# Kernel tuning notes

Hardware: AMD Instinct MI355X
Metric: run time of the kernel (lower is better)

The kernel has to match this reference:

```python
import jax, jax.numpy as jnp
import numpy as np
from jax import lax

B, D, T = 8, 768, 1024
H = 8
DH = D // H  # 96
FF = 4 * D
NUM_BUCKETS = 320
HALF = NUM_BUCKETS // 2      # 160
SMALL = HALF // 2            # 80
MAX_DIST = 800
CONV_K = 31
ATTN_SCALE = 32.0


def setup_inputs() -> dict:
    key = jax.random.key(0)
    ks = jax.random.split(key, 32)
    n = lambda i, shape, s=0.02: jax.random.normal(ks[i], shape, dtype=jnp.float32) * s
    return {
        "x": jax.random.normal(ks[0], (B, D, T), dtype=jnp.float32),
        # ff1
        "w_ff1a": n(1, (D, FF)), "b_ff1a": jnp.zeros((FF,)),
        "w_ff1b": n(2, (FF, D)), "b_ff1b": jnp.zeros((D,)),
        # attention
        "w_qkv": n(3, (D, 3 * D)), "b_qkv": jnp.zeros((3 * D,)),
        "w_out": n(4, (D, D)), "b_out": jnp.zeros((D,)),
        # gated relative position bias
        "rel_embed": n(5, (NUM_BUCKETS, H), 1.0),
        "gate_u": n(6, (H, DH)), "gate_w": n(7, (H, DH)),
        "gate_scale": jnp.ones((H,)),
        # conv module
        "gn1_w": jnp.ones((D,)), "gn1_b": jnp.zeros((D,)),
        "pw1_w": n(8, (2 * D, D)), "pw1_b": jnp.zeros((2 * D,)),
        "dw_w": n(9, (D, CONV_K)), "dw_b": jnp.zeros((D,)),
        "gn2_w": jnp.ones((D,)), "gn2_b": jnp.zeros((D,)),
        "pw2_w": n(10, (D, D)), "pw2_b": jnp.zeros((D,)),
        # ff2
        "w_ff2a": n(11, (D, FF)), "b_ff2a": jnp.zeros((FF,)),
        "w_ff2b": n(12, (FF, D)), "b_ff2b": jnp.zeros((D,)),
    }


def _rel_buckets(seq_len):
    pos = jnp.arange(seq_len)
    rp = pos[None, :] - pos[:, None]              # [T, T]
    sign = (rp >= 0).astype(jnp.int32)
    ra = jnp.abs(rp)
    is_small = ra < SMALL
    rc = jnp.maximum(ra, 1)
    log_ratio = jnp.log(rc.astype(jnp.float32) / SMALL) / np.float32(np.log(MAX_DIST / SMALL))
    log_pos = SMALL + (log_ratio * (HALF - SMALL)).astype(jnp.int32)  # trunc toward zero like .long()
    log_pos = jnp.minimum(log_pos, HALF - 1)
    bucket = jnp.where(is_small, ra, log_pos) + sign * HALF
    return jnp.clip(bucket, 0, NUM_BUCKETS - 1)


def _groupnorm1(xc, w, b, eps=1e-5):
    # GroupNorm(1, C): normalize over (C, T) per sample; xc: [B, C, T]
    m = xc.mean(axis=(1, 2), keepdims=True)
    v = xc.var(axis=(1, 2), keepdims=True)
    return (xc - m) * lax.rsqrt(v + eps) * w[None, :, None] + b[None, :, None]


def reference(x, w_ff1a, b_ff1a, w_ff1b, b_ff1b, w_qkv, b_qkv, w_out, b_out,
              rel_embed, gate_u, gate_w, gate_scale,
              gn1_w, gn1_b, pw1_w, pw1_b, dw_w, dw_b, gn2_w, gn2_b, pw2_w, pw2_b,
              w_ff2a, b_ff2a, w_ff2b, b_ff2b):
    b_, d_, t_ = x.shape
    s = jnp.swapaxes(x, 1, 2)                          # [B, T, D]

    ff = lambda t, wa, ba, wb, bb: jax.nn.gelu(t @ wa + ba, approximate=False) @ wb + bb
    s = s + 0.5 * ff(s, w_ff1a, b_ff1a, w_ff1b, b_ff1b)

    qkv = (s @ w_qkv + b_qkv).reshape(b_, t_, 3, H, DH)
    q = jnp.swapaxes(qkv[:, :, 0], 1, 2)               # [B, H, T, DH]
    k = jnp.swapaxes(qkv[:, :, 1], 1, 2)
    v = jnp.swapaxes(qkv[:, :, 2], 1, 2)

    # WavLM-style rescaled scores
    scores = jnp.einsum('bhtd,bhsd->bhts', q / ATTN_SCALE, k)
    scores = (scores - scores.max(axis=-1, keepdims=True)) * ATTN_SCALE
    scores = scores / np.float32(np.sqrt(DH))

    # gated relative position bias
    buckets = _rel_buckets(t_)                          # [T, T]
    dtab = jnp.transpose(rel_embed[buckets], (2, 0, 1))[None]  # [1, H, T, T]
    g_u = jax.nn.sigmoid(jnp.einsum('bhtd,hd->bht', q, gate_u))[..., None]  # [B,H,T,1]
    g_r = jax.nn.sigmoid(jnp.einsum('bhtd,hd->bht', q, gate_w))[..., None]
    r_tilde = gate_scale[None, :, None, None] * g_r * dtab
    rel_bias = dtab + g_u * dtab + (1.0 - g_u) * r_tilde

    probs = jax.nn.softmax(scores + rel_bias, axis=-1)
    attn = jnp.einsum('bhts,bhsd->bhtd', probs, v)
    attn = jnp.swapaxes(attn, 1, 2).reshape(b_, t_, d_)
    s = s + attn @ w_out + b_out

    # conv module
    c = jnp.swapaxes(s, 1, 2)                           # [B, D, T]
    h = _groupnorm1(c, gn1_w, gn1_b)
    h = jnp.einsum('od,bdt->bot', pw1_w, h) + pw1_b[None, :, None]  # 1x1 conv -> [B, 2D, T]
    a, g = jnp.split(h, 2, axis=1)
    h = a * jax.nn.sigmoid(g)                           # GLU over channels
    h = lax.conv_general_dilated(h, dw_w[:, None, :], (1,), [(CONV_K // 2, CONV_K // 2)],
                                 feature_group_count=d_,
                                 dimension_numbers=('NCH', 'OIH', 'NCH')) + dw_b[None, :, None]
    h = jax.nn.silu(_groupnorm1(h, gn2_w, gn2_b))
    h = jnp.einsum('od,bdt->bot', pw2_w, h) + pw2_b[None, :, None]
    c = c + h

    ct = jnp.swapaxes(c, 1, 2)
    s = ct + 0.5 * ff(ct, w_ff2a, b_ff2a, w_ff2b, b_ff2b)
    return jnp.swapaxes(s, 1, 2)                        # [B, D, T]
```

## Files before the change

kernel.cpp:

```cpp
#include <hip/hip_runtime.h>
#include <hip/hip_bf16.h>
#include <cstdint>

typedef __attribute__((ext_vector_type(8))) __bf16 bf16x8;
typedef __attribute__((ext_vector_type(4))) float f32x4;
typedef unsigned short u16t;

constexpr int Bn = 8, Dn = 768, Tn = 1024, Hn = 8, DHn = 96, FFn = 3072;
constexpr int BT = Bn * Tn;
constexpr float INV_SQRT_DH = 0.10206207261596575f;

#define GLDS16(gp, lp) __builtin_amdgcn_global_load_lds( \
    (__attribute__((address_space(1))) unsigned int*)(uintptr_t)(gp), \
    (__attribute__((address_space(3))) unsigned int*)(uintptr_t)(lp), 16, 0, 0)

__global__ void k_prep(const float* __restrict__ w_ff1a, const float* __restrict__ w_ff1b,
                       const float* __restrict__ w_qkv, const float* __restrict__ w_out,
                       const float* __restrict__ w_ff2a, const float* __restrict__ w_ff2b,
                       const float* __restrict__ pw1_w, const float* __restrict__ pw2_w,
                       const float* __restrict__ rel_embed,
                       __hip_bfloat16* __restrict__ Wf1a, __hip_bfloat16* __restrict__ Wf1b,
                       __hip_bfloat16* __restrict__ Wqkv, __hip_bfloat16* __restrict__ Wout,
                       __hip_bfloat16* __restrict__ Wf2a, __hip_bfloat16* __restrict__ Wf2b,
                       __hip_bfloat16* __restrict__ Wpw1, __hip_bfloat16* __restrict__ Wpw2,
                       float* __restrict__ rel_tab) {
  __shared__ float t[32][33];
  const int tid = threadIdx.x;
  int bid = blockIdx.x;

  const float* tsrc = nullptr;
  __hip_bfloat16* tdst = nullptr;
  int K = 0, N = 0;
  if (bid < 2304) { tsrc = w_ff1a; tdst = Wf1a; K = 768; N = 3072; }
  else if ((bid -= 2304) < 2304) { tsrc = w_ff1b; tdst = Wf1b; K = 3072; N = 768; }
  else if ((bid -= 2304) < 1728) { tsrc = w_qkv; tdst = Wqkv; K = 768; N = 2304; }
  else if ((bid -= 1728) < 576)  { tsrc = w_out; tdst = Wout; K = 768; N = 768; }
  else if ((bid -= 576) < 2304)  { tsrc = w_ff2a; tdst = Wf2a; K = 768; N = 3072; }
  else if ((bid -= 2304) < 2304) { tsrc = w_ff2b; tdst = Wf2b; K = 3072; N = 768; }
  else {
    bid -= 2304;
    if (bid < 1152) {
      int i4 = bid * 1024 + tid * 4;
      int n = i4 / 768, k = i4 - n * 768;
      int on = (n >> 1) + (n & 1) * 768;
      float4 v = *(const float4*)(pw1_w + (size_t)on * 768 + k);
      __hip_bfloat16* d = Wpw1 + i4;
      d[0] = __float2bfloat16(v.x); d[1] = __float2bfloat16(v.y);
      d[2] = __float2bfloat16(v.z); d[3] = __float2bfloat16(v.w);
    } else if ((bid -= 1152) < 576) {
      int i4 = bid * 1024 + tid * 4;
      float4 v = *(const float4*)(pw2_w + i4);
      __hip_bfloat16* d = Wpw2 + i4;
      d[0] = __float2bfloat16(v.x); d[1] = __float2bfloat16(v.y);
      d[2] = __float2bfloat16(v.z); d[3] = __float2bfloat16(v.w);
    } else {
      bid -= 576;
      int dd = bid * 256 + tid;
      if (dd < 2047) {
        int d = dd - 1023;
        int sign = d >= 0 ? 1 : 0;
        int ra = d < 0 ? -d : d;
        int base;
        if (ra < 80) base = ra;
        else {
          float lr = logf((float)ra / 80.0f) / 2.3025851f;
          int lp = 80 + (int)(lr * 80.0f);
          base = lp < 159 ? lp : 159;
        }
        int bucket = base + sign * 160;
        if (bucket < 0) bucket = 0;
        if (bucket > 319) bucket = 319;
        for (int h = 0; h < 8; ++h)
          rel_tab[h * 2047 + dd] = rel_embed[bucket * 8 + h];
      }
    }
    return;
  }
  int nb32 = N / 32;
  int nb = (bid % nb32) * 32, kb = (bid / nb32) * 32;
  int tx = tid & 31, ty = tid >> 5;
  for (int i = ty; i < 32; i += 8)
    t[i][tx] = tsrc[(size_t)(kb + i) * N + nb + tx];
  __syncthreads();
  for (int i = ty; i < 32; i += 8)
    tdst[(size_t)(nb + i) * K + kb + tx] = __float2bfloat16(t[tx][i]);
}

__global__ void k_tin(const float* __restrict__ x, float* __restrict__ s,
                      __hip_bfloat16* __restrict__ sb) {
  __shared__ float t[32][33];
  int b = blockIdx.z;
  int t0 = blockIdx.x * 32, d0 = blockIdx.y * 32;
  int tx = threadIdx.x, ty = threadIdx.y;
  for (int i = ty; i < 32; i += 8)
    t[i][tx] = x[((size_t)b * Dn + d0 + i) * Tn + t0 + tx];
  __syncthreads();
  for (int i = ty; i < 32; i += 8) {
    float v = t[tx][i];
    size_t o = (size_t)(b * Tn + t0 + i) * Dn + d0 + tx;
    s[o] = v;
    sb[o] = __float2bfloat16(v);
  }
}

__global__ void k_tout(const float* __restrict__ s, float* __restrict__ out) {
  __shared__ float t[32][33];
  int b = blockIdx.z;
  int t0 = blockIdx.x * 32, d0 = blockIdx.y * 32;
  int tx = threadIdx.x, ty = threadIdx.y;
  for (int i = ty; i < 32; i += 8)
    t[i][tx] = s[(size_t)(b * Tn + t0 + i) * Dn + d0 + tx];
  __syncthreads();
  for (int i = ty; i < 32; i += 8)
    out[((size_t)b * Dn + d0 + i) * Tn + t0 + tx] = t[tx][i];
}

__global__ void k_vtrans(const __hip_bfloat16* __restrict__ qkv,
                         __hip_bfloat16* __restrict__ VT) {
  __shared__ __hip_bfloat16 t[32][33];
  int bh = blockIdx.z;
  int b = bh >> 3, h = bh & 7;
  int t0 = blockIdx.x * 32, d0 = blockIdx.y * 32;
  int tx = threadIdx.x, ty = threadIdx.y;
  for (int i = ty; i < 32; i += 8)
    t[i][tx] = qkv[(size_t)(b * Tn + t0 + i) * 2304 + 1536 + h * 96 + d0 + tx];
  __syncthreads();
  for (int i = ty; i < 32; i += 8)
    VT[((size_t)bh * 96 + d0 + i) * Tn + t0 + tx] = t[tx][i];
}

enum { EPI_BIAS = 0, EPI_GELU = 1, EPI_HALF_RES = 2, EPI_RES = 3, EPI_GLU = 4 };

template <int BM, int BN, int EPI>
__global__ __launch_bounds__(256)
void k_gemm(const __hip_bfloat16* __restrict__ A, const __hip_bfloat16* __restrict__ Bt,
            const float* __restrict__ bias, const float* __restrict__ resid,
            float* __restrict__ outF, __hip_bfloat16* __restrict__ outB,
            int M, int N, int K) {
  constexpr int MI = BM / 32;
  constexpr int NI = BN / 32;
  __shared__ __align__(16) __hip_bfloat16 lA[2][BM * 32];
  __shared__ __align__(16) __hip_bfloat16 lB[2][BN * 32];
  const int tid = threadIdx.x;
  const int lane = tid & 63, wv = tid >> 6;
  const int g = lane >> 4, c15 = lane & 15;
  const int gx = gridDim.x;
  const int nwg = gx * gridDim.y;
  const int orig = blockIdx.y * gx + blockIdx.x;
  const int q = nwg >> 3, rr = nwg & 7;
  const int xcd = orig & 7, idx = orig >> 3;
  const int wg = (xcd < rr ? xcd * (q + 1) : rr * (q + 1) + (xcd - rr) * q) + idx;
  const int m0 = (wg / gx) * BM, n0 = (wg % gx) * BN;
  const int wm = (wv >> 1) * (BM / 2), wn = (wv & 1) * (BN / 2);

  const int srow = lane >> 2, scol = (lane & 3) * 8;

  f32x4 acc[MI][NI] = {};

  auto stage = [&](int buf, int kt) {
#pragma unroll
    for (int c = 0; c < BM / 64; ++c) {
      int cid = wv * (BM / 64) + c;
      GLDS16(A + (size_t)(m0 + cid * 16 + srow) * K + kt + scol, &lA[buf][cid * 512]);
    }
#pragma unroll
    for (int c = 0; c < BN / 64; ++c) {
      int cid = wv * (BN / 64) + c;
      GLDS16(Bt + (size_t)(n0 + cid * 16 + srow) * K + kt + scol, &lB[buf][cid * 512]);
    }
  };

  const int nt = K >> 5;
  stage(0, 0);
  __syncthreads();
  int cur = 0;
  for (int t = 0; t < nt; ++t) {
    if (t + 1 < nt) stage(cur ^ 1, (t + 1) * 32);
    bf16x8 af[MI], bfr[NI];
#pragma unroll
    for (int i = 0; i < MI; ++i)
      af[i] = *(const bf16x8*)&lA[cur][(wm + i * 16 + c15) * 32 + g * 8];
#pragma unroll
    for (int j = 0; j < NI; ++j)
      bfr[j] = *(const bf16x8*)&lB[cur][(wn + j * 16 + c15) * 32 + g * 8];
#pragma unroll
    for (int i = 0; i < MI; ++i)
#pragma unroll
      for (int j = 0; j < NI; ++j)
        acc[i][j] = __builtin_amdgcn_mfma_f32_16x16x32_bf16(af[i], bfr[j], acc[i][j], 0, 0, 0);
    __syncthreads();
    cur ^= 1;
  }

#pragma unroll
  for (int i = 0; i < MI; ++i) {
    int row0 = m0 + wm + i * 16 + g * 4;
#pragma unroll
    for (int j = 0; j < NI; ++j) {
      int col = n0 + wn + j * 16 + c15;
      int bcol = (EPI == EPI_GLU) ? ((col >> 1) + (col & 1) * 768) : col;
      float bb = bias[bcol];
#pragma unroll
      for (int r = 0; r < 4; ++r) {
        int row = row0 + r;
        float v = acc[i][j][r] + bb;
        if (EPI == EPI_GELU) v = 0.5f * v * (1.0f + erff(v * 0.70710678118f));
        else if (EPI == EPI_HALF_RES) v = resid[(size_t)row * N + col] + 0.5f * v;
        else if (EPI == EPI_RES) v = resid[(size_t)row * N + col] + v;
        if (EPI == EPI_GLU) {
          float partner = __shfl_xor(v, 1);
          if (!(c15 & 1))
            outF[(size_t)row * (N >> 1) + (col >> 1)] =
                v * (1.0f / (1.0f + __expf(-partner)));
        } else {
          size_t o = (size_t)row * N + col;
          if (outF) outF[o] = v;
          if (outB) outB[o] = __float2bfloat16(v);
        }
      }
    }
  }
}

__global__ __launch_bounds__(256)
void k_attn(const __hip_bfloat16* __restrict__ qkv, const __hip_bfloat16* __restrict__ VT,
            const float* __restrict__ rel_tab,
            const float* __restrict__ gate_u, const float* __restrict__ gate_w,
            const float* __restrict__ gate_scale, __hip_bfloat16* __restrict__ ao) {
  __shared__ __align__(16) char smem[48128];
  __hip_bfloat16* kT = (__hip_bfloat16*)smem;
  __hip_bfloat16* vT = (__hip_bfloat16*)(smem + 13312);
  __hip_bfloat16* qT = (__hip_bfloat16*)(smem + 30208);
  __hip_bfloat16* pT = (__hip_bfloat16*)(smem + 30208);
  float* relLocal = (float*)(smem + 43520);
  float* cRow = (float*)(smem + 47872);

  const int tid = threadIdx.x, lane = tid & 63, wv = tid >> 6;
  const int g = lane >> 4, c15 = lane & 15;
  const int orig = blockIdx.y * 16 + blockIdx.x;
  const int wg = (orig & 7) * 128 + (orig >> 3);
  const int qt = wg & 15;
  const int bh = wg >> 4;
  const int b = bh >> 3, h = bh & 7;
  const int t0 = qt * 64;

  for (int i = tid; i < 1087; i += 256)
    relLocal[i] = rel_tab[h * 2047 + i + 960 - t0];

  {
    int r = tid >> 2, q4 = tid & 3;
    const __hip_bfloat16* src = qkv + (size_t)(b * Tn + t0 + r) * 2304 + h * 96 + q4 * 24;
    uint4 v0 = *(const uint4*)(src);
    uint4 v1 = *(const uint4*)(src + 8);
    uint4 v2 = *(const uint4*)(src + 16);
    *(uint4*)&qT[r * 104 + q4 * 24] = v0;
    *(uint4*)&qT[r * 104 + q4 * 24 + 8] = v1;
    *(uint4*)&qT[r * 104 + q4 * 24 + 16] = v2;
  }
  __syncthreads();

  if (tid < 64) {
    float du = 0.f, dw = 0.f;
#pragma unroll
    for (int c = 0; c < 12; ++c) {
      bf16x8 qv = *(const bf16x8*)&qT[tid * 104 + c * 8];
#pragma unroll
      for (int e = 0; e < 8; ++e) {
        float f = (float)qv[e];
        du += f * gate_u[h * 96 + c * 8 + e];
        dw += f * gate_w[h * 96 + c * 8 + e];
      }
    }
    float gu = 1.0f / (1.0f + __expf(-du));
    float gr = 1.0f / (1.0f + __expf(-dw));
    cRow[tid] = 1.0f + gu + (1.0f - gu) * gate_scale[h] * gr;
  }

  bf16x8 aQ[3];
#pragma unroll
  for (int c = 0; c < 3; ++c)
    aQ[c] = *(const bf16x8*)&qT[(wv * 16 + c15) * 104 + c * 32 + g * 8];
  __syncthreads();

  float crw[4];
#pragma unroll
  for (int r = 0; r < 4; ++r) crw[r] = cRow[wv * 16 + g * 4 + r];

  float mrow[4], ssum[4];
#pragma unroll
  for (int r = 0; r < 4; ++r) { mrow[r] = -1e30f; ssum[r] = 0.0f; }
  f32x4 accO[6] = {};

  for (int kt = 0; kt < 16; ++kt) {
    {
      int r = tid >> 2, q4 = tid & 3;
      const __hip_bfloat16* ks =
          qkv + (size_t)(b * Tn + kt * 64 + r) * 2304 + 768 + h * 96 + q4 * 24;
      uint4 k0 = *(const uint4*)(ks);
      uint4 k1 = *(const uint4*)(ks + 8);
      uint4 k2 = *(const uint4*)(ks + 16);
      *(uint4*)&kT[r * 104 + q4 * 24] = k0;
      *(uint4*)&kT[r * 104 + q4 * 24 + 8] = k1;
      *(uint4*)&kT[r * 104 + q4 * 24 + 16] = k2;
    }
    {
#pragma unroll
      for (int i = 0; i < 3; ++i) {
        int cid = i * 256 + tid;
        int row = cid >> 3, ch = cid & 7;
        const __hip_bfloat16* vs = VT + ((size_t)bh * 96 + row) * Tn + kt * 64 + ch * 8;
        *(uint4*)&vT[row * 88 + ch * 8] = *(const uint4*)vs;
      }
    }
    __syncthreads();

    f32x4 accS[4];
    __builtin_amdgcn_s_setprio(1);
#pragma unroll
    for (int j = 0; j < 4; ++j) {
      f32x4 s = {};
#pragma unroll
      for (int c = 0; c < 3; ++c) {
        bf16x8 bk = *(const bf16x8*)&kT[(j * 16 + c15) * 104 + c * 32 + g * 8];
        s = __builtin_amdgcn_mfma_f32_16x16x32_bf16(aQ[c], bk, s, 0, 0, 0);
      }
      accS[j] = s;
    }
    __builtin_amdgcn_s_setprio(0);

    float sv[4][4];
    const int tq_off = wv * 16 + g * 4;
#pragma unroll
    for (int j = 0; j < 4; ++j) {
      int tk = kt * 64 + j * 16 + c15;
#pragma unroll
      for (int r = 0; r < 4; ++r)
        sv[j][r] = accS[j][r] * INV_SQRT_DH + crw[r] * relLocal[tk - (tq_off + r) + 63];
    }

    float pmax[4];
#pragma unroll
    for (int r = 0; r < 4; ++r) {
      float m = fmaxf(fmaxf(sv[0][r], sv[1][r]), fmaxf(sv[2][r], sv[3][r]));
#pragma unroll
      for (int off = 1; off < 16; off <<= 1) m = fmaxf(m, __shfl_xor(m, off, 64));
      pmax[r] = m;
    }
    int grow = (pmax[0] > mrow[0] + 8.0f) | (pmax[1] > mrow[1] + 8.0f) |
               (pmax[2] > mrow[2] + 8.0f) | (pmax[3] > mrow[3] + 8.0f);
    if (__any(grow)) {
#pragma unroll
      for (int r = 0; r < 4; ++r) {
        float newm = fmaxf(mrow[r], pmax[r]);
        float sc = __expf(mrow[r] - newm);
        ssum[r] *= sc;
        mrow[r] = newm;
#pragma unroll
        for (int f = 0; f < 6; ++f) accO[f][r] *= sc;
      }
    }
#pragma unroll
    for (int r = 0; r < 4; ++r) {
      float ps = 0.0f;
#pragma unroll
      for (int j = 0; j < 4; ++j) {
        float p = __expf(sv[j][r] - mrow[r]);
        sv[j][r] = p;
        ps += p;
      }
#pragma unroll
      for (int off = 1; off < 16; off <<= 1) ps += __shfl_xor(ps, off, 64);
      ssum[r] += ps;
    }

#pragma unroll
    for (int j = 0; j < 4; ++j)
#pragma unroll
      for (int r = 0; r < 4; ++r)
        pT[wv * 1408 + (g * 4 + r) * 88 + j * 16 + c15] = __float2bfloat16(sv[j][r]);

    bf16x8 ap0 = *(const bf16x8*)&pT[wv * 1408 + c15 * 88 + g * 8];
    bf16x8 ap1 = *(const bf16x8*)&pT[wv * 1408 + c15 * 88 + 32 + g * 8];
    __builtin_amdgcn_s_setprio(1);
#pragma unroll
    for (int f = 0; f < 6; ++f) {
      bf16x8 bv0 = *(const bf16x8*)&vT[(f * 16 + c15) * 88 + g * 8];
      bf16x8 bv1 = *(const bf16x8*)&vT[(f * 16 + c15) * 88 + 32 + g * 8];
      accO[f] = __builtin_amdgcn_mfma_f32_16x16x32_bf16(ap0, bv0, accO[f], 0, 0, 0);
      accO[f] = __builtin_amdgcn_mfma_f32_16x16x32_bf16(ap1, bv1, accO[f], 0, 0, 0);
    }
    __builtin_amdgcn_s_setprio(0);
    __syncthreads();
  }

  float inv[4];
#pragma unroll
  for (int r = 0; r < 4; ++r) inv[r] = 1.0f / ssum[r];
#pragma unroll
  for (int f = 0; f < 6; ++f)
#pragma unroll
    for (int r = 0; r < 4; ++r) {
      int trow = t0 + wv * 16 + g * 4 + r;
      ao[(size_t)(b * Tn + trow) * Dn + h * 96 + f * 16 + c15] =
          __float2bfloat16(accO[f][r] * inv[r]);
    }
}

__global__ __launch_bounds__(256)
void k_dwconv(const float* __restrict__ in, const float* __restrict__ w,
              const float* __restrict__ bias, float* __restrict__ out) {
  __shared__ float tile[94][64];
  __shared__ float wt[64][31];
  __shared__ float bt[64];
  int b = blockIdx.z, t0 = blockIdx.x * 64, d0 = blockIdx.y * 64;
  int tid = threadIdx.x;
  for (int e = tid; e < 94 * 64; e += 256) {
    int rr = e >> 6, dd = e & 63;
    int t = t0 - 15 + rr;
    tile[rr][dd] = (t >= 0 && t < Tn) ? in[(size_t)(b * Tn + t) * Dn + d0 + dd] : 0.0f;
  }
  for (int e = tid; e < 64 * 31; e += 256) {
    int dd = e / 31, k = e - dd * 31;
    wt[dd][k] = w[(d0 + dd) * 31 + k];
  }
  if (tid < 64) bt[tid] = bias[d0 + tid];
  __syncthreads();
  for (int o = tid; o < 64 * 64; o += 256) {
    int tt = o >> 6, dd = o & 63;
    float s = bt[dd];
#pragma unroll
    for (int k = 0; k < 31; ++k) s += tile[tt + k][dd] * wt[dd][k];
    out[(size_t)(b * Tn + t0 + tt) * Dn + d0 + dd] = s;
  }
}

__global__ void k_gn_part(const float* __restrict__ x, float* __restrict__ part) {
  int b = blockIdx.y, c = blockIdx.x, tid = threadIdx.x;
  const float4* p = (const float4*)(x + (size_t)b * (Dn * Tn) + c * 8192);
  float s = 0.f, q = 0.f;
  for (int i = tid; i < 2048; i += 256) {
    float4 v = p[i];
    s += v.x + v.y + v.z + v.w;
    q += v.x * v.x + v.y * v.y + v.z * v.z + v.w * v.w;
  }
  for (int off = 1; off < 64; off <<= 1) {
    s += __shfl_xor(s, off, 64);
    q += __shfl_xor(q, off, 64);
  }
  __shared__ float ls[4], lq[4];
  int lane = tid & 63, wv = tid >> 6;
  if (lane == 0) { ls[wv] = s; lq[wv] = q; }
  __syncthreads();
  if (tid == 0) {
    part[(b * 96 + c) * 2] = ls[0] + ls[1] + ls[2] + ls[3];
    part[(b * 96 + c) * 2 + 1] = lq[0] + lq[1] + lq[2] + lq[3];
  }
}

__global__ void k_gn_final(const float* __restrict__ part, float* __restrict__ stats) {
  int b = blockIdx.x, tid = threadIdx.x;
  float s = 0.f, q = 0.f;
  if (tid < 96) { s = part[(b * 96 + tid) * 2]; q = part[(b * 96 + tid) * 2 + 1]; }
  for (int off = 1; off < 64; off <<= 1) {
    s += __shfl_xor(s, off, 64);
    q += __shfl_xor(q, off, 64);
  }
  __shared__ float ls[2], lq[2];
  int lane = tid & 63, wv = tid >> 6;
  if (lane == 0) { ls[wv] = s; lq[wv] = q; }
  __syncthreads();
  if (tid == 0) {
    const float N = (float)(Dn * Tn);
    float mean = (ls[0] + ls[1]) / N;
    float var = (lq[0] + lq[1]) / N - mean * mean;
    stats[b * 2] = mean;
    stats[b * 2 + 1] = rsqrtf(var + 1e-5f);
  }
}

template <bool SILU>
__global__ void k_gn_apply(const float* __restrict__ x, const float* __restrict__ stats,
                           const float* __restrict__ w, const float* __restrict__ bb,
                           __hip_bfloat16* __restrict__ out) {
  int i4 = (blockIdx.x * 256 + threadIdx.x) * 4;
  if (i4 >= BT * Dn) return;
  int row = i4 / Dn, d = i4 - row * Dn;
  int b = row >> 10;
  float mean = stats[b * 2], rstd = stats[b * 2 + 1];
  float4 xv = *(const float4*)(x + i4);
  float4 wv4 = *(const float4*)(w + d);
  float4 bv4 = *(const float4*)(bb + d);
  float v0 = (xv.x - mean) * rstd * wv4.x + bv4.x;
  float v1 = (xv.y - mean) * rstd * wv4.y + bv4.y;
  float v2 = (xv.z - mean) * rstd * wv4.z + bv4.z;
  float v3 = (xv.w - mean) * rstd * wv4.w + bv4.w;
  if (SILU) {
    v0 = v0 / (1.0f + __expf(-v0));
    v1 = v1 / (1.0f + __expf(-v1));
    v2 = v2 / (1.0f + __expf(-v2));
    v3 = v3 / (1.0f + __expf(-v3));
  }
  union { ushort4 u; __hip_bfloat16 h[4]; } o;
  o.h[0] = __float2bfloat16(v0);
  o.h[1] = __float2bfloat16(v1);
  o.h[2] = __float2bfloat16(v2);
  o.h[3] = __float2bfloat16(v3);
  *(ushort4*)(out + i4) = o.u;
}

extern "C" void kernel_launch(void* const* d_in, const int* in_sizes, int n_in,
                              void* d_out, int out_size, void* d_ws, size_t ws_size,
                              hipStream_t stream) {
  const float* x         = (const float*)d_in[0];
  const float* w_ff1a    = (const float*)d_in[1];
  const float* b_ff1a    = (const float*)d_in[2];
  const float* w_ff1b    = (const float*)d_in[3];
  const float* b_ff1b    = (const float*)d_in[4];
  const float* w_qkv     = (const float*)d_in[5];
  const float* b_qkv     = (const float*)d_in[6];
  const float* w_out     = (const float*)d_in[7];
  const float* b_out     = (const float*)d_in[8];
  const float* rel_embed = (const float*)d_in[9];
  const float* gate_u    = (const float*)d_in[10];
  const float* gate_w    = (const float*)d_in[11];
  const float* gate_sc   = (const float*)d_in[12];
  const float* gn1_w     = (const float*)d_in[13];
  const float* gn1_b     = (const float*)d_in[14];
  const float* pw1_w     = (const float*)d_in[15];
  const float* pw1_b     = (const float*)d_in[16];
  const float* dw_w      = (const float*)d_in[17];
  const float* dw_b      = (const float*)d_in[18];
  const float* gn2_w     = (const float*)d_in[19];
  const float* gn2_b     = (const float*)d_in[20];
  const float* pw2_w     = (const float*)d_in[21];
  const float* pw2_b     = (const float*)d_in[22];
  const float* w_ff2a    = (const float*)d_in[23];
  const float* b_ff2a    = (const float*)d_in[24];
  const float* w_ff2b    = (const float*)d_in[25];
  const float* b_ff2b    = (const float*)d_in[26];

  char* ws = (char*)d_ws;
  size_t off = 0;
  auto alloc = [&](size_t bytes) {
    void* p = ws + off;
    off = (off + bytes + 255) & ~(size_t)255;
    return p;
  };

  float* SA = (float*)alloc((size_t)BT * Dn * 4);
  float* SB = (float*)alloc((size_t)BT * Dn * 4);
  __hip_bfloat16* ABF = (__hip_bfloat16*)alloc((size_t)BT * Dn * 2);
  void* BIG = alloc((size_t)BT * FFn * 2);
  void* QKV = alloc((size_t)BT * 2304 * 2);
  __hip_bfloat16* Wf1a = (__hip_bfloat16*)alloc((size_t)Dn * FFn * 2);
  __hip_bfloat16* Wf1b = (__hip_bfloat16*)alloc((size_t)Dn * FFn * 2);
  __hip_bfloat16* Wqkv = (__hip_bfloat16*)alloc((size_t)Dn * 2304 * 2);
  __hip_bfloat16* Wout = (__hip_bfloat16*)alloc((size_t)Dn * Dn * 2);
  __hip_bfloat16* Wpw1 = (__hip_bfloat16*)alloc((size_t)1536 * Dn * 2);
  __hip_bfloat16* Wpw2 = (__hip_bfloat16*)alloc((size_t)Dn * Dn * 2);
  __hip_bfloat16* Wf2a = (__hip_bfloat16*)alloc((size_t)Dn * FFn * 2);
  __hip_bfloat16* Wf2b = (__hip_bfloat16*)alloc((size_t)Dn * FFn * 2);
  float* RELT  = (float*)alloc(8 * 2047 * 4);
  float* GPART = (float*)alloc(8 * 96 * 2 * 4);
  float* GSTAT = (float*)alloc(8 * 2 * 4);
  __hip_bfloat16* VT = (__hip_bfloat16*)BIG;
  float* GLUF = (float*)QKV;
  float* DWO = (float*)d_out;

  dim3 blk32(32, 8);

  const int PREP_BLOCKS = 2304 + 2304 + 1728 + 576 + 2304 + 2304 + 1152 + 576 + 8;
  k_prep<<<PREP_BLOCKS, 256, 0, stream>>>(
      w_ff1a, w_ff1b, w_qkv, w_out, w_ff2a, w_ff2b, pw1_w, pw2_w, rel_embed,
      Wf1a, Wf1b, Wqkv, Wout, Wf2a, Wf2b, Wpw1, Wpw2, RELT);

  k_tin<<<dim3(Tn / 32, Dn / 32, Bn), blk32, 0, stream>>>(x, SA, ABF);

  k_gemm<128, 128, EPI_GELU><<<dim3(FFn / 128, BT / 128), 256, 0, stream>>>(
      ABF, Wf1a, b_ff1a, nullptr, nullptr, (__hip_bfloat16*)BIG, BT, FFn, Dn);
  k_gemm<64, 128, EPI_HALF_RES><<<dim3(Dn / 128, BT / 64), 256, 0, stream>>>(
      (__hip_bfloat16*)BIG, Wf1b, b_ff1b, SA, SB, ABF, BT, Dn, FFn);

  k_gemm<128, 128, EPI_BIAS><<<dim3(2304 / 128, BT / 128), 256, 0, stream>>>(
      ABF, Wqkv, b_qkv, nullptr, nullptr, (__hip_bfloat16*)QKV, BT, 2304, Dn);

  k_vtrans<<<dim3(Tn / 32, 3, 64), blk32, 0, stream>>>((const __hip_bfloat16*)QKV, VT);

  k_attn<<<dim3(16, 64), 256, 0, stream>>>((const __hip_bfloat16*)QKV, VT, RELT,
                                           gate_u, gate_w, gate_sc, ABF);

  k_gemm<64, 128, EPI_RES><<<dim3(Dn / 128, BT / 64), 256, 0, stream>>>(
      ABF, Wout, b_out, SB, SA, nullptr, BT, Dn, Dn);

  k_gn_part<<<dim3(96, 8), 256, 0, stream>>>(SA, GPART);
  k_gn_final<<<8, 128, 0, stream>>>(GPART, GSTAT);
  k_gn_apply<false><<<(BT * Dn / 4 + 255) / 256, 256, 0, stream>>>(SA, GSTAT, gn1_w, gn1_b, ABF);

  k_gemm<64, 128, EPI_GLU><<<dim3(1536 / 128, BT / 64), 256, 0, stream>>>(
      ABF, Wpw1, pw1_b, nullptr, GLUF, nullptr, BT, 1536, Dn);
  k_dwconv<<<dim3(Tn / 64, Dn / 64, Bn), 256, 0, stream>>>(GLUF, dw_w, dw_b, DWO);
  k_gn_part<<<dim3(96, 8), 256, 0, stream>>>(DWO, GPART);
  k_gn_final<<<8, 128, 0, stream>>>(GPART, GSTAT);
  k_gn_apply<true><<<(BT * Dn / 4 + 255) / 256, 256, 0, stream>>>(DWO, GSTAT, gn2_w, gn2_b, ABF);

  k_gemm<64, 128, EPI_RES><<<dim3(Dn / 128, BT / 64), 256, 0, stream>>>(
      ABF, Wpw2, pw2_b, SA, SB, ABF, BT, Dn, Dn);

  k_gemm<128, 128, EPI_GELU><<<dim3(FFn / 128, BT / 128), 256, 0, stream>>>(
      ABF, Wf2a, b_ff2a, nullptr, nullptr, (__hip_bfloat16*)BIG, BT, FFn, Dn);
  k_gemm<64, 128, EPI_HALF_RES><<<dim3(Dn / 128, BT / 64), 256, 0, stream>>>(
      (__hip_bfloat16*)BIG, Wf2b, b_ff2b, SB, SA, nullptr, BT, Dn, FFn);

  k_tout<<<dim3(Tn / 32, Dn / 32, Bn), blk32, 0, stream>>>(SA, (float*)d_out);
}
```

Baseline: 627.3 us.

## Double-buffer K/V tiles in attention kernel with register prefetch

```diff
diff --git a/kernel.cpp b/kernel.cpp
--- a/kernel.cpp
+++ b/kernel.cpp
@@ -227,13 +227,11 @@
             const float* __restrict__ rel_tab,
             const float* __restrict__ gate_u, const float* __restrict__ gate_w,
             const float* __restrict__ gate_scale, __hip_bfloat16* __restrict__ ao) {
-  __shared__ __align__(16) char smem[48128];
-  __hip_bfloat16* kT = (__hip_bfloat16*)smem;
-  __hip_bfloat16* vT = (__hip_bfloat16*)(smem + 13312);
-  __hip_bfloat16* qT = (__hip_bfloat16*)(smem + 30208);
-  __hip_bfloat16* pT = (__hip_bfloat16*)(smem + 30208);
-  float* relLocal = (float*)(smem + 43520);
-  float* cRow = (float*)(smem + 47872);
+  __shared__ __align__(16) char smem[78336];
+  __hip_bfloat16* qT = (__hip_bfloat16*)(smem + 60416);
+  __hip_bfloat16* pT = (__hip_bfloat16*)(smem + 60416);
+  float* relLocal = (float*)(smem + 73728);
+  float* cRow = (float*)(smem + 78080);
 
   const int tid = threadIdx.x, lane = tid & 63, wv = tid >> 6;
   const int g = lane >> 4, c15 = lane & 15;
@@ -244,18 +242,40 @@
   const int b = bh >> 3, h = bh & 7;
   const int t0 = qt * 64;
 
+  const int kr_ = tid >> 2, kq4 = tid & 3;
+  const __hip_bfloat16* kgbase =
+      qkv + (size_t)(b * Tn + kr_) * 2304 + 768 + h * 96 + kq4 * 24;
+  const int vrow0 = tid >> 3, vch = tid & 7;
+  const int vrow1 = (256 + tid) >> 3, vrow2 = (512 + tid) >> 3;
+  const __hip_bfloat16* vgbase = VT + (size_t)bh * 96 * Tn;
+
   for (int i = tid; i < 1087; i += 256)
     relLocal[i] = rel_tab[h * 2047 + i + 960 - t0];
 
   {
-    int r = tid >> 2, q4 = tid & 3;
-    const __hip_bfloat16* src = qkv + (size_t)(b * Tn + t0 + r) * 2304 + h * 96 + q4 * 24;
+    const __hip_bfloat16* src = qkv + (size_t)(b * Tn + t0 + kr_) * 2304 + h * 96 + kq4 * 24;
     uint4 v0 = *(const uint4*)(src);
     uint4 v1 = *(const uint4*)(src + 8);
     uint4 v2 = *(const uint4*)(src + 16);
-    *(uint4*)&qT[r * 104 + q4 * 24] = v0;
-    *(uint4*)&qT[r * 104 + q4 * 24 + 8] = v1;
-    *(uint4*)&qT[r * 104 + q4 * 24 + 16] = v2;
+    *(uint4*)&qT[kr_ * 104 + kq4 * 24] = v0;
+    *(uint4*)&qT[kr_ * 104 + kq4 * 24 + 8] = v1;
+    *(uint4*)&qT[kr_ * 104 + kq4 * 24 + 16] = v2;
+  }
+  {
+    __hip_bfloat16* kT0 = (__hip_bfloat16*)smem;
+    __hip_bfloat16* vT0 = (__hip_bfloat16*)(smem + 13312);
+    uint4 k0 = *(const uint4*)(kgbase);
+    uint4 k1 = *(const uint4*)(kgbase + 8);
+    uint4 k2 = *(const uint4*)(kgbase + 16);
+    *(uint4*)&kT0[kr_ * 104 + kq4 * 24] = k0;
+    *(uint4*)&kT0[kr_ * 104 + kq4 * 24 + 8] = k1;
+    *(uint4*)&kT0[kr_ * 104 + kq4 * 24 + 16] = k2;
+    uint4 w0 = *(const uint4*)(vgbase + (size_t)vrow0 * Tn + vch * 8);
+    uint4 w1 = *(const uint4*)(vgbase + (size_t)vrow1 * Tn + vch * 8);
+    uint4 w2 = *(const uint4*)(vgbase + (size_t)vrow2 * Tn + vch * 8);
+    *(uint4*)&vT0[vrow0 * 88 + vch * 8] = w0;
+    *(uint4*)&vT0[vrow1 * 88 + vch * 8] = w1;
+    *(uint4*)&vT0[vrow2 * 88 + vch * 8] = w2;
   }
   __syncthreads();
 
@@ -291,28 +311,22 @@
   for (int r = 0; r < 4; ++r) { mrow[r] = -1e30f; ssum[r] = 0.0f; }
   f32x4 accO[6] = {};
 
+  int cur = 0;
   for (int kt = 0; kt < 16; ++kt) {
-    {
-      int r = tid >> 2, q4 = tid & 3;
-      const __hip_bfloat16* ks =
-          qkv + (size_t)(b * Tn + kt * 64 + r) * 2304 + 768 + h * 96 + q4 * 24;
-      uint4 k0 = *(const uint4*)(ks);
-      uint4 k1 = *(const uint4*)(ks + 8);
-      uint4 k2 = *(const uint4*)(ks + 16);
-      *(uint4*)&kT[r * 104 + q4 * 24] = k0;
-      *(uint4*)&kT[r * 104 + q4 * 24 + 8] = k1;
-      *(uint4*)&kT[r * 104 + q4 * 24 + 16] = k2;
-    }
-    {
-#pragma unroll
-      for (int i = 0; i < 3; ++i) {
-        int cid = i * 256 + tid;
-        int row = cid >> 3, ch = cid & 7;
-        const __hip_bfloat16* vs = VT + ((size_t)bh * 96 + row) * Tn + kt * 64 + ch * 8;
-        *(uint4*)&vT[row * 88 + ch * 8] = *(const uint4*)vs;
-      }
-    }
-    __syncthreads();
+    __hip_bfloat16* kT = (__hip_bfloat16*)(smem + cur * 30208);
+    __hip_bfloat16* vT = (__hip_bfloat16*)(smem + cur * 30208 + 13312);
+
+    uint4 nk0, nk1, nk2, nv0, nv1, nv2;
+    if (kt < 15) {
+      const __hip_bfloat16* kg = kgbase + (size_t)(kt + 1) * 64 * 2304;
+      nk0 = *(const uint4*)(kg);
+      nk1 = *(const uint4*)(kg + 8);
+      nk2 = *(const uint4*)(kg + 16);
+      const __hip_bfloat16* vg = vgbase + (kt + 1) * 64;
+      nv0 = *(const uint4*)(vg + (size_t)vrow0 * Tn + vch * 8);
+      nv1 = *(const uint4*)(vg + (size_t)vrow1 * Tn + vch * 8);
+      nv2 = *(const uint4*)(vg + (size_t)vrow2 * Tn + vch * 8);
+    }
 
     f32x4 accS[4];
     __builtin_amdgcn_s_setprio(1);
@@ -390,7 +404,19 @@
       accO[f] = __builtin_amdgcn_mfma_f32_16x16x32_bf16(ap1, bv1, accO[f], 0, 0, 0);
     }
     __builtin_amdgcn_s_setprio(0);
+
+    if (kt < 15) {
+      __hip_bfloat16* kTn = (__hip_bfloat16*)(smem + (cur ^ 1) * 30208);
+      __hip_bfloat16* vTn = (__hip_bfloat16*)(smem + (cur ^ 1) * 30208 + 13312);
+      *(uint4*)&kTn[kr_ * 104 + kq4 * 24] = nk0;
+      *(uint4*)&kTn[kr_ * 104 + kq4 * 24 + 8] = nk1;
+      *(uint4*)&kTn[kr_ * 104 + kq4 * 24 + 16] = nk2;
+      *(uint4*)&vTn[vrow0 * 88 + vch * 8] = nv0;
+      *(uint4*)&vTn[vrow1 * 88 + vch * 8] = nv1;
+      *(uint4*)&vTn[vrow2 * 88 + vch * 8] = nv2;
+    }
     __syncthreads();
+    cur ^= 1;
   }
 
   float inv[4];
```

After: 624.2 us. Within noise of the previous version (-0.5%).

## Double attention query tile to 128 rows and prefetch next K/V into registers

Applied to the files above, without the earlier changes.

```diff
diff --git a/kernel.cpp b/kernel.cpp
--- a/kernel.cpp
+++ b/kernel.cpp
@@ -227,39 +227,44 @@
             const float* __restrict__ rel_tab,
             const float* __restrict__ gate_u, const float* __restrict__ gate_w,
             const float* __restrict__ gate_scale, __hip_bfloat16* __restrict__ ao) {
-  __shared__ __align__(16) char smem[48128];
+  __shared__ __align__(16) char smem[61952];
   __hip_bfloat16* kT = (__hip_bfloat16*)smem;
   __hip_bfloat16* vT = (__hip_bfloat16*)(smem + 13312);
   __hip_bfloat16* qT = (__hip_bfloat16*)(smem + 30208);
   __hip_bfloat16* pT = (__hip_bfloat16*)(smem + 30208);
-  float* relLocal = (float*)(smem + 43520);
-  float* cRow = (float*)(smem + 47872);
+  float* relLocal = (float*)(smem + 56832);
+  float* cRow = (float*)(smem + 61440);
 
   const int tid = threadIdx.x, lane = tid & 63, wv = tid >> 6;
   const int g = lane >> 4, c15 = lane & 15;
-  const int orig = blockIdx.y * 16 + blockIdx.x;
-  const int wg = (orig & 7) * 128 + (orig >> 3);
-  const int qt = wg & 15;
-  const int bh = wg >> 4;
+  const int orig = blockIdx.y * 8 + blockIdx.x;
+  const int wg = (orig & 7) * 64 + (orig >> 3);
+  const int qt = wg & 7;
+  const int bh = wg >> 3;
   const int b = bh >> 3, h = bh & 7;
-  const int t0 = qt * 64;
-
-  for (int i = tid; i < 1087; i += 256)
-    relLocal[i] = rel_tab[h * 2047 + i + 960 - t0];
+  const int t0 = qt * 128;
+
+  const int kr_ = tid >> 2, kq4 = tid & 3;
+  const __hip_bfloat16* kgbase =
+      qkv + (size_t)(b * Tn + kr_) * 2304 + 768 + h * 96 + kq4 * 24;
+  const int vrow0 = tid >> 3, vch = tid & 7;
+  const int vrow1 = (256 + tid) >> 3, vrow2 = (512 + tid) >> 3;
+  const __hip_bfloat16* vgbase = VT + (size_t)bh * 96 * Tn;
+
+  for (int i = tid; i < 1151; i += 256)
+    relLocal[i] = rel_tab[h * 2047 + i + 896 - t0];
 
   {
-    int r = tid >> 2, q4 = tid & 3;
-    const __hip_bfloat16* src = qkv + (size_t)(b * Tn + t0 + r) * 2304 + h * 96 + q4 * 24;
-    uint4 v0 = *(const uint4*)(src);
-    uint4 v1 = *(const uint4*)(src + 8);
-    uint4 v2 = *(const uint4*)(src + 16);
-    *(uint4*)&qT[r * 104 + q4 * 24] = v0;
-    *(uint4*)&qT[r * 104 + q4 * 24 + 8] = v1;
-    *(uint4*)&qT[r * 104 + q4 * 24 + 16] = v2;
-  }
-  __syncthreads();
-
-  if (tid < 64) {
+    int qr = tid >> 1, qh = tid & 1;
+    const __hip_bfloat16* src =
+        qkv + (size_t)(b * Tn + t0 + qr) * 2304 + h * 96 + qh * 48;
+#pragma unroll
+    for (int k = 0; k < 6; ++k)
+      *(uint4*)&qT[qr * 104 + qh * 48 + k * 8] = *(const uint4*)(src + k * 8);
+  }
+  __syncthreads();
+
+  if (tid < 128) {
     float du = 0.f, dw = 0.f;
 #pragma unroll
     for (int c = 0; c < 12; ++c) {
@@ -276,134 +281,175 @@
     cRow[tid] = 1.0f + gu + (1.0f - gu) * gate_scale[h] * gr;
   }
 
-  bf16x8 aQ[3];
-#pragma unroll
-  for (int c = 0; c < 3; ++c)
-    aQ[c] = *(const bf16x8*)&qT[(wv * 16 + c15) * 104 + c * 32 + g * 8];
-  __syncthreads();
-
-  float crw[4];
-#pragma unroll
-  for (int r = 0; r < 4; ++r) crw[r] = cRow[wv * 16 + g * 4 + r];
-
-  float mrow[4], ssum[4];
-#pragma unroll
-  for (int r = 0; r < 4; ++r) { mrow[r] = -1e30f; ssum[r] = 0.0f; }
-  f32x4 accO[6] = {};
+  bf16x8 aQ[2][3];
+#pragma unroll
+  for (int u = 0; u < 2; ++u)
+#pragma unroll
+    for (int c = 0; c < 3; ++c)
+      aQ[u][c] = *(const bf16x8*)&qT[(wv * 32 + u * 16 + c15) * 104 + c * 32 + g * 8];
+  __syncthreads();
+
+  float crw[2][4];
+#pragma unroll
+  for (int u = 0; u < 2; ++u)
+#pragma unroll
+    for (int r = 0; r < 4; ++r)
+      crw[u][r] = cRow[wv * 32 + u * 16 + g * 4 + r];
+
+  float mrow[2][4], ssum[2][4];
+#pragma unroll
+  for (int u = 0; u < 2; ++u)
+#pragma unroll
+    for (int r = 0; r < 4; ++r) { mrow[u][r] = -1e30f; ssum[u][r] = 0.0f; }
+  f32x4 accO[2][6] = {};
+
+  uint4 nk0 = *(const uint4*)(kgbase);
+  uint4 nk1 = *(const uint4*)(kgbase + 8);
+  uint4 nk2 = *(const uint4*)(kgbase + 16);
+  uint4 nv0 = *(const uint4*)(vgbase + (size_t)vrow0 * Tn + vch * 8);
+  uint4 nv1 = *(const uint4*)(vgbase + (size_t)vrow1 * Tn + vch * 8);
+  uint4 nv2 = *(const uint4*)(vgbase + (size_t)vrow2 * Tn + vch * 8);
 
   for (int kt = 0; kt < 16; ++kt) {
-    {
-      int r = tid >> 2, q4 = tid & 3;
-      const __hip_bfloat16* ks =
-          qkv + (size_t)(b * Tn + kt * 64 + r) * 2304 + 768 + h * 96 + q4 * 24;
-      uint4 k0 = *(const uint4*)(ks);
-      uint4 k1 = *(const uint4*)(ks + 8);
-      uint4 k2 = *(const uint4*)(ks + 16);
-      *(uint4*)&kT[r * 104 + q4 * 24] = k0;
-      *(uint4*)&kT[r * 104 + q4 * 24 + 8] = k1;
-      *(uint4*)&kT[r * 104 + q4 * 24 + 16] = k2;
-    }
-    {
-#pragma unroll
-      for (int i = 0; i < 3; ++i) {
-        int cid = i * 256 + tid;
-        int row = cid >> 3, ch = cid & 7;
-        const __hip_bfloat16* vs = VT + ((size_t)bh * 96 + row) * Tn + kt * 64 + ch * 8;
-        *(uint4*)&vT[row * 88 + ch * 8] = *(const uint4*)vs;
-      }
-    }
+    *(uint4*)&kT[kr_ * 104 + kq4 * 24] = nk0;
+    *(uint4*)&kT[kr_ * 104 + kq4 * 24 + 8] = nk1;
+    *(uint4*)&kT[kr_ * 104 + kq4 * 24 + 16] = nk2;
+    *(uint4*)&vT[vrow0 * 88 + vch * 8] = nv0;
+    *(uint4*)&vT[vrow1 * 88 + vch * 8] = nv1;
+    *(uint4*)&vT[vrow2 * 88 + vch * 8] = nv2;
     __syncthreads();
 
-    f32x4 accS[4];
+    if (kt < 15) {
+      const __hip_bfloat16* kg = kgbase + (size_t)(kt + 1) * 64 * 2304;
+      nk0 = *(const uint4*)(kg);
+      nk1 = *(const uint4*)(kg + 8);
+      nk2 = *(const uint4*)(kg + 16);
+      const __hip_bfloat16* vg = vgbase + (kt + 1) * 64;
+      nv0 = *(const uint4*)(vg + (size_t)vrow0 * Tn + vch * 8);
+      nv1 = *(const uint4*)(vg + (size_t)vrow1 * Tn + vch * 8);
+      nv2 = *(const uint4*)(vg + (size_t)vrow2 * Tn + vch * 8);
+    }
+
+    f32x4 accS[2][4];
     __builtin_amdgcn_s_setprio(1);
 #pragma unroll
     for (int j = 0; j < 4; ++j) {
-      f32x4 s = {};
-#pragma unroll
-      for (int c = 0; c < 3; ++c) {
-        bf16x8 bk = *(const bf16x8*)&kT[(j * 16 + c15) * 104 + c * 32 + g * 8];
-        s = __builtin_amdgcn_mfma_f32_16x16x32_bf16(aQ[c], bk, s, 0, 0, 0);
-      }
-      accS[j] = s;
+      bf16x8 bk0 = *(const bf16x8*)&kT[(j * 16 + c15) * 104 + g * 8];
+      bf16x8 bk1 = *(const bf16x8*)&kT[(j * 16 + c15) * 104 + 32 + g * 8];
+      bf16x8 bk2 = *(const bf16x8*)&kT[(j * 16 + c15) * 104 + 64 + g * 8];
+#pragma unroll
+      for (int u = 0; u < 2; ++u) {
+        f32x4 s = {};
+        s = __builtin_amdgcn_mfma_f32_16x16x32_bf16(aQ[u][0], bk0, s, 0, 0, 0);
+        s = __builtin_amdgcn_mfma_f32_16x16x32_bf16(aQ[u][1], bk1, s, 0, 0, 0);
+        s = __builtin_amdgcn_mfma_f32_16x16x32_bf16(aQ[u][2], bk2, s, 0, 0, 0);
+        accS[u][j] = s;
+      }
     }
     __builtin_amdgcn_s_setprio(0);
 
-    float sv[4][4];
-    const int tq_off = wv * 16 + g * 4;
-#pragma unroll
-    for (int j = 0; j < 4; ++j) {
-      int tk = kt * 64 + j * 16 + c15;
+    float sv[2][4][4];
+    const int tq0 = wv * 32 + g * 4;
+#pragma unroll
+    for (int u = 0; u < 2; ++u)
+#pragma unroll
+      for (int j = 0; j < 4; ++j) {
+        int tk = kt * 64 + j * 16 + c15;
+#pragma unroll
+        for (int r = 0; r < 4; ++r)
+          sv[u][j][r] = accS[u][j][r] * INV_SQRT_DH +
+                        crw[u][r] * relLocal[tk - (tq0 + u * 16 + r) + 127];
+      }
+
+    float pmax[2][4];
+#pragma unroll
+    for (int u = 0; u < 2; ++u)
+#pragma unroll
+      for (int r = 0; r < 4; ++r) {
+        float m = fmaxf(fmaxf(sv[u][0][r], sv[u][1][r]), fmaxf(sv[u][2][r], sv[u][3][r]));
+#pragma unroll
+        for (int off = 1; off < 16; off <<= 1) m = fmaxf(m, __shfl_xor(m, off, 64));
+        pmax[u][r] = m;
+      }
+    int grow = 0;
+#pragma unroll
+    for (int u = 0; u < 2; ++u)
 #pragma unroll
       for (int r = 0; r < 4; ++r)
-        sv[j][r] = accS[j][r] * INV_SQRT_DH + crw[r] * relLocal[tk - (tq_off + r) + 63];
-    }
-
-    float pmax[4];
-#pragma unroll
-    for (int r = 0; r < 4; ++r) {
-      float m = fmaxf(fmaxf(sv[0][r], sv[1][r]), fmaxf(sv[2][r], sv[3][r]));
-#pragma unroll
-      for (int off = 1; off < 16; off <<= 1) m = fmaxf(m, __shfl_xor(m, off, 64));
-      pmax[r] = m;
-    }
-    int grow = (pmax[0] > mrow[0] + 8.0f) | (pmax[1] > mrow[1] + 8.0f) |
-               (pmax[2] > mrow[2] + 8.0f) | (pmax[3] > mrow[3] + 8.0f);
+        grow |= (pmax[u][r] > mrow[u][r] + 8.0f);
     if (__any(grow)) {
 #pragma unroll
+      for (int u = 0; u < 2; ++u)
+#pragma unroll
+        for (int r = 0; r < 4; ++r) {
+          float newm = fmaxf(mrow[u][r], pmax[u][r]);
+          float sc = __expf(mrow[u][r] - newm);
+          ssum[u][r] *= sc;
+          mrow[u][r] = newm;
+#pragma unroll
+          for (int f = 0; f < 6; ++f) accO[u][f][r] *= sc;
+        }
+    }
+#pragma unroll
+    for (int u = 0; u < 2; ++u)
+#pragma unroll
       for (int r = 0; r < 4; ++r) {
-        float newm = fmaxf(mrow[r], pmax[r]);
-        float sc = __expf(mrow[r] - newm);
-        ssum[r] *= sc;
-        mrow[r] = newm;
-#pragma unroll
-        for (int f = 0; f < 6; ++f) accO[f][r] *= sc;
-      }
-    }
-#pragma unroll
-    for (int r = 0; r < 4; ++r) {
-      float ps = 0.0f;
-#pragma unroll
-      for (int j = 0; j < 4; ++j) {
-        float p = __expf(sv[j][r] - mrow[r]);
-        sv[j][r] = p;
-        ps += p;
-      }
-#pragma unroll
-      for (int off = 1; off < 16; off <<= 1) ps += __shfl_xor(ps, off, 64);
-      ssum[r] += ps;
-    }
-
-#pragma unroll
-    for (int j = 0; j < 4; ++j)
-#pragma unroll
-      for (int r = 0; r < 4; ++r)
-        pT[wv * 1408 + (g * 4 + r) * 88 + j * 16 + c15] = __float2bfloat16(sv[j][r]);
-
-    bf16x8 ap0 = *(const bf16x8*)&pT[wv * 1408 + c15 * 88 + g * 8];
-    bf16x8 ap1 = *(const bf16x8*)&pT[wv * 1408 + c15 * 88 + 32 + g * 8];
+        float ps = 0.0f;
+#pragma unroll
+        for (int j = 0; j < 4; ++j) {
+          float p = __expf(sv[u][j][r] - mrow[u][r]);
+          sv[u][j][r] = p;
+          ps += p;
+        }
+#pragma unroll
+        for (int off = 1; off < 16; off <<= 1) ps += __shfl_xor(ps, off, 64);
+        ssum[u][r] += ps;
+      }
+
+#pragma unroll
+    for (int u = 0; u < 2; ++u)
+#pragma unroll
+      for (int j = 0; j < 4; ++j)
+#pragma unroll
+        for (int r = 0; r < 4; ++r)
+          pT[wv * 2816 + (u * 16 + g * 4 + r) * 88 + j * 16 + c15] =
+              __float2bfloat16(sv[u][j][r]);
+
+    bf16x8 ap[2][2];
+#pragma unroll
+    for (int u = 0; u < 2; ++u) {
+      ap[u][0] = *(const bf16x8*)&pT[wv * 2816 + (u * 16 + c15) * 88 + g * 8];
+      ap[u][1] = *(const bf16x8*)&pT[wv * 2816 + (u * 16 + c15) * 88 + 32 + g * 8];
+    }
     __builtin_amdgcn_s_setprio(1);
 #pragma unroll
     for (int f = 0; f < 6; ++f) {
       bf16x8 bv0 = *(const bf16x8*)&vT[(f * 16 + c15) * 88 + g * 8];
       bf16x8 bv1 = *(const bf16x8*)&vT[(f * 16 + c15) * 88 + 32 + g * 8];
-      accO[f] = __builtin_amdgcn_mfma_f32_16x16x32_bf16(ap0, bv0, accO[f], 0, 0, 0);
-      accO[f] = __builtin_amdgcn_mfma_f32_16x16x32_bf16(ap1, bv1, accO[f], 0, 0, 0);
+#pragma unroll
+      for (int u = 0; u < 2; ++u) {
+        accO[u][f] = __builtin_amdgcn_mfma_f32_16x16x32_bf16(ap[u][0], bv0, accO[u][f], 0, 0, 0);
+        accO[u][f] = __builtin_amdgcn_mfma_f32_16x16x32_bf16(ap[u][1], bv1, accO[u][f], 0, 0, 0);
+      }
     }
     __builtin_amdgcn_s_setprio(0);
     __syncthreads();
   }
 
-  float inv[4];
-#pragma unroll
-  for (int r = 0; r < 4; ++r) inv[r] = 1.0f / ssum[r];
-#pragma unroll
-  for (int f = 0; f < 6; ++f)
-#pragma unroll
-    for (int r = 0; r < 4; ++r) {
-      int trow = t0 + wv * 16 + g * 4 + r;
-      ao[(size_t)(b * Tn + trow) * Dn + h * 96 + f * 16 + c15] =
-          __float2bfloat16(accO[f][r] * inv[r]);
-    }
+#pragma unroll
+  for (int u = 0; u < 2; ++u) {
+    float inv[4];
+#pragma unroll
+    for (int r = 0; r < 4; ++r) inv[r] = 1.0f / ssum[u][r];
+#pragma unroll
+    for (int f = 0; f < 6; ++f)
+#pragma unroll
+      for (int r = 0; r < 4; ++r) {
+        int trow = t0 + wv * 32 + u * 16 + g * 4 + r;
+        ao[(size_t)(b * Tn + trow) * Dn + h * 96 + f * 16 + c15] =
+            __float2bfloat16(accO[u][f][r] * inv[r]);
+      }
+  }
 }
 
 __global__ __launch_bounds__(256)
@@ -586,8 +632,8 @@
 
   k_vtrans<<<dim3(Tn / 32, 3, 64), blk32, 0, stream>>>((const __hip_bfloat16*)QKV, VT);
 
-  k_attn<<<dim3(16, 64), 256, 0, stream>>>((const __hip_bfloat16*)QKV, VT, RELT,
-                                           gate_u, gate_w, gate_sc, ABF);
+  k_attn<<<dim3(8, 64), 256, 0, stream>>>((const __hip_bfloat16*)QKV, VT, RELT,
+                                          gate_u, gate_w, gate_sc, ABF);
 
   k_gemm<64, 128, EPI_RES><<<dim3(Dn / 128, BT / 64), 256, 0, stream>>>(
       ABF, Wout, b_out, SB, SA, nullptr, BT, Dn, Dn);
```

Measured after the change: 641.5 us. +2.3%, slower.
